# Optimization experiments

Measured on AMD Instinct MI355X. Metric: run time of the kernel, lower is better.

The kernel has to match this reference:

```python
import jax, jax.numpy as jnp
import numpy as np

B = 64          # molecules per batch
N_ATOMS = 16    # atoms per molecule (uniform -> torch.split == reshape)
DIM = 128
N = B * N_ATOMS # 1024 total atoms
N_FP = 10000
N_BOND_FP = 10000
EPS = 1e-12     # F.normalize default eps


def setup_inputs() -> dict:
    key = jax.random.key(0)
    ks = jax.random.split(key, 12)
    s = 1.0 / np.sqrt(DIM)
    # block-diagonal structure: molecule id per atom
    mol = jnp.arange(N) // N_ATOMS
    block = mol[:, None] == mol[None, :]
    fingerprints = jax.random.randint(ks[0], (N,), 0, N_FP, dtype=jnp.int32)
    # pad() fills off-block with 0.0; in-block: sparse binary bonds
    adjacency = jnp.where(block, (jax.random.uniform(ks[1], (N, N)) < 0.3).astype(jnp.float32), 0.0)
    # pad_MPO() fills off-block with index 0 (which still embeds to a real row!)
    bond_index = jnp.where(block, jax.random.randint(ks[2], (N, N), 0, N_BOND_FP, dtype=jnp.int32), 0)
    return {
        "fingerprints": fingerprints,
        "adjacency": adjacency,
        "bond_index": bond_index,
        "E_fp": jax.random.normal(ks[3], (N_FP, DIM), jnp.float32),
        "E_bond": jax.random.normal(ks[4], (N_BOND_FP, DIM), jnp.float32),
        "W_fp": jax.random.normal(ks[5], (DIM, DIM), jnp.float32) * s,
        "b_fp": jnp.zeros((DIM,), jnp.float32),
        "W_out0": jax.random.normal(ks[6], (DIM, DIM), jnp.float32) * s,
        "b_out0": jnp.zeros((DIM,), jnp.float32),
        "W_out1": jax.random.normal(ks[7], (DIM, DIM), jnp.float32) * s,
        "b_out1": jnp.zeros((DIM,), jnp.float32),
        "W_prop": jax.random.normal(ks[8], (DIM, 1), jnp.float32) * s,
        "b_prop": jnp.zeros((1,), jnp.float32),
    }


def _l2norm(x, axis):
    n = jnp.sqrt(jnp.sum(x * x, axis=axis, keepdims=True))
    return x / jnp.maximum(n, EPS)


def reference(fingerprints, adjacency, bond_index, E_fp, E_bond, W_fp, b_fp,
              W_out0, b_out0, W_out1, b_out1, W_prop, b_prop):
    # MPS: atom embeddings + one round of dense (block-diag) message passing
    mps = E_fp[fingerprints]                                   # [N, d]
    contri = jax.nn.relu(mps @ W_fp + b_fp)                    # [N, d]
    mps = mps + adjacency @ contri                             # [N, d]
    mps = _l2norm(mps, axis=1)                                 # F.normalize(., 2, 1)
    # MPO: embedding of the padded [N, N] bond index -> [N, N, d]
    mpo = E_bond[bond_index]                                   # [N, N, d]
    mpo = _l2norm(mpo, axis=1)                                 # normalize over 2nd atom axis
    # tmp[c, b] = sum_a mps[a, c] * mpo[a, b, c]
    tmp = jnp.einsum('ac,abc->cb', mps, mpo)                   # [d, N]
    # uniform molecular_sizes -> torch.split == reshape
    info = tmp.reshape(DIM, B, N_ATOMS)                        # [d, B, n]
    fv = mps.reshape(B, N_ATOMS, DIM)                          # [B, n, d]
    tn = jnp.einsum('dmn,mnd->md', info, fv)                   # [B, d]
    x = jax.nn.relu(tn @ W_out0 + b_out0)
    x = jax.nn.relu(x @ W_out1 + b_out1)
    return x @ W_prop + b_prop                                 # [B, 1]
```

## Files before the change

### kernel.cpp

```cpp
#include <hip/hip_runtime.h>
#include <math.h>

#define DIM_   128
#define NAT_   16
#define NTOT_  1024
#define BMOL_  64
#define OFFB_  1008.0f
#define EPSF_  1e-12f

__global__ __launch_bounds__(1024) void kA(const int* __restrict__ fp,
                                           const float* __restrict__ Efp,
                                           const float* __restrict__ Wfp,
                                           const float* __restrict__ bfp,
                                           const float* __restrict__ adj,
                                           const int* __restrict__ bidx,
                                           const float* __restrict__ Ebond,
                                           float* __restrict__ TnP_g,
                                           float* __restrict__ SbP_g,
                                           float* __restrict__ Mb_g) {
    const int b = blockIdx.x;
    const int m = b >> 1, h = b & 1, base = m * NAT_;
    const int t = threadIdx.x;
    const int c = t & 127;
    const int s = t >> 7;
    const int j0 = 2 * s, j1 = 2 * s + 1;
    const int jg = 8 * h + s;

    __shared__ float mpsS[NAT_][DIM_];
    __shared__ float conS[NAT_][DIM_];
    __shared__ float adjS[NAT_][NAT_];
    __shared__ int   bSh[8][NAT_];
    __shared__ float redS[NAT_][2];
    __shared__ float nrmS[NAT_];
    __shared__ float sb8[8][DIM_];
    __shared__ float tnp8[8][DIM_];

    {
        int j = t >> 7, cc = t & 127;
        mpsS[j][cc] = Efp[(size_t)fp[base + j] * DIM_ + cc];
        j += 8;
        mpsS[j][cc] = Efp[(size_t)fp[base + j] * DIM_ + cc];
    }
    if (t < 256) {
        const int j = t >> 4, i = t & 15;
        adjS[j][i] = adj[(size_t)(base + j) * NTOT_ + base + i];
    } else if (t < 384) {
        const int tt = t - 256, j = tt >> 4, i = tt & 15;
        bSh[j][i] = bidx[(size_t)(base + 8 * h + j) * NTOT_ + base + i];
    }
    __syncthreads();

    float a0 = bfp[c];
    float a1 = a0;
    #pragma unroll 8
    for (int k = 0; k < DIM_; ++k) {
        const float w = Wfp[(size_t)k * DIM_ + c];
        a0 += mpsS[j0][k] * w;
        a1 += mpsS[j1][k] * w;
    }
    conS[j0][c] = fmaxf(a0, 0.0f);
    conS[j1][c] = fmaxf(a1, 0.0f);
    __syncthreads();

    float ms0 = mpsS[j0][c], ms1 = mpsS[j1][c];
    #pragma unroll
    for (int i = 0; i < NAT_; ++i) {
        const float cv = conS[i][c];
        ms0 += adjS[j0][i] * cv;
        ms1 += adjS[j1][i] * cv;
    }
    float v0 = ms0 * ms0, v1 = ms1 * ms1;
    #pragma unroll
    for (int o = 32; o > 0; o >>= 1) {
        v0 += __shfl_xor(v0, o, 64);
        v1 += __shfl_xor(v1, o, 64);
    }
    const int half = (t >> 6) & 1;
    if ((t & 63) == 0) { redS[j0][half] = v0; redS[j1][half] = v1; }
    __syncthreads();
    if (t < NAT_) nrmS[t] = fmaxf(sqrtf(redS[t][0] + redS[t][1]), EPSF_);
    __syncthreads();
    mpsS[j0][c] = ms0 / nrmS[j0];
    mpsS[j1][c] = ms1 / nrmS[j1];
    __syncthreads();

    {
        const float e0 = Ebond[c];
        float nsq = OFFB_ * e0 * e0;
        int bb[NAT_];
        #pragma unroll
        for (int i = 0; i < NAT_; ++i) bb[i] = bSh[s][i];
        float ev[NAT_];
        #pragma unroll
        for (int i = 0; i < NAT_; ++i) ev[i] = Ebond[(size_t)bb[i] * DIM_ + c];
        #pragma unroll
        for (int i = 0; i < NAT_; ++i) nsq += ev[i] * ev[i];
        const float msc = mpsS[jg][c] / fmaxf(sqrtf(nsq), EPSF_);
        float tj = 0.0f;
        #pragma unroll
        for (int i = 0; i < NAT_; ++i) tj += ev[i] * mpsS[i][c];
        sb8[s][c]  = msc;
        tnp8[s][c] = msc * tj;
    }
    __syncthreads();

    if (s == 0) {
        float Tn = 0.0f, Sb = 0.0f;
        #pragma unroll
        for (int q = 0; q < 8; ++q) { Tn += tnp8[q][c]; Sb += sb8[q][c]; }
        TnP_g[(size_t)b * DIM_ + c] = Tn;
        SbP_g[(size_t)b * DIM_ + c] = Sb;
    } else if (s == 1 && h == 0) {
        float mb = 0.0f;
        #pragma unroll
        for (int i = 0; i < NAT_; ++i) mb += mpsS[i][c];
        Mb_g[(size_t)m * DIM_ + c] = mb;
    }
}

__global__ __launch_bounds__(512) void kB(const float* __restrict__ Ebond,
                                          const float* __restrict__ TnP_g,
                                          const float* __restrict__ SbP_g,
                                          const float* __restrict__ Mb_g,
                                          const float* __restrict__ W0, const float* __restrict__ b0,
                                          const float* __restrict__ W1, const float* __restrict__ b1,
                                          const float* __restrict__ Wp, const float* __restrict__ bp,
                                          float* __restrict__ out) {
    const int m = blockIdx.x;
    const int t = threadIdx.x;
    const int c = t & 127;
    const int s = t >> 7;
    __shared__ float w4[4][DIM_];
    __shared__ float vS[DIM_];
    __shared__ float tnS[DIM_];
    __shared__ float r2[2];

    {
        float S = 0.0f;
        float tv[32];
        #pragma unroll
        for (int r = 0; r < 32; ++r)
            tv[r] = SbP_g[(size_t)(s * 32 + r) * DIM_ + c];
        #pragma unroll
        for (int r = 0; r < 32; ++r) S += tv[r];
        w4[s][c] = S;
    }
    __syncthreads();
    if (s == 0) {
        const float Sall = w4[0][c] + w4[1][c] + w4[2][c] + w4[3][c];
        const float Sb_m = SbP_g[(size_t)(2 * m) * DIM_ + c] + SbP_g[(size_t)(2 * m + 1) * DIM_ + c];
        const float Tn_m = TnP_g[(size_t)(2 * m) * DIM_ + c] + TnP_g[(size_t)(2 * m + 1) * DIM_ + c];
        vS[c] = Tn_m + Ebond[c] * (Sall - Sb_m) * Mb_g[(size_t)m * DIM_ + c];
    }
    __syncthreads();

    {
        float a1 = 0.0f;
        #pragma unroll 8
        for (int r = 0; r < 32; ++r) {
            const int d = s * 32 + r;
            a1 += vS[d] * W0[(size_t)d * DIM_ + c];
        }
        w4[s][c] = a1;
    }
    __syncthreads();
    if (s == 0) tnS[c] = fmaxf(w4[0][c] + w4[1][c] + w4[2][c] + w4[3][c] + b0[c], 0.0f);
    __syncthreads();
    {
        float a2 = 0.0f;
        #pragma unroll 8
        for (int r = 0; r < 32; ++r) {
            const int d = s * 32 + r;
            a2 += tnS[d] * W1[(size_t)d * DIM_ + c];
        }
        w4[s][c] = a2;
    }
    __syncthreads();
    if (s == 0) {
        const float x1 = fmaxf(w4[0][c] + w4[1][c] + w4[2][c] + w4[3][c] + b1[c], 0.0f);
        float vv = x1 * Wp[c];
        #pragma unroll
        for (int o = 32; o > 0; o >>= 1) vv += __shfl_xor(vv, o, 64);
        if ((c & 63) == 0) r2[c >> 6] = vv;
    }
    __syncthreads();
    if (t == 0) out[m] = r2[0] + r2[1] + bp[0];
}

extern "C" void kernel_launch(void* const* d_in, const int* in_sizes, int n_in,
                              void* d_out, int out_size, void* d_ws, size_t ws_size,
                              hipStream_t stream) {
    const int*   fingerprints = (const int*)  d_in[0];
    const float* adjacency    = (const float*)d_in[1];
    const int*   bond_index   = (const int*)  d_in[2];
    const float* E_fp         = (const float*)d_in[3];
    const float* E_bond       = (const float*)d_in[4];
    const float* W_fp         = (const float*)d_in[5];
    const float* b_fp         = (const float*)d_in[6];
    const float* W_out0       = (const float*)d_in[7];
    const float* b_out0       = (const float*)d_in[8];
    const float* W_out1       = (const float*)d_in[9];
    const float* b_out1       = (const float*)d_in[10];
    const float* W_prop       = (const float*)d_in[11];
    const float* b_prop       = (const float*)d_in[12];
    float* out = (float*)d_out;

    float* ws = (float*)d_ws;
    const size_t PD = (size_t)128 * DIM_;
    float* TnP = ws;
    float* SbP = ws + PD;
    float* Mb  = ws + 2 * PD;

    kA<<<128, 1024, 0, stream>>>(fingerprints, E_fp, W_fp, b_fp, adjacency, bond_index,
                                 E_bond, TnP, SbP, Mb);
    kB<<<BMOL_, 512, 0, stream>>>(E_bond, TnP, SbP, Mb,
                                  W_out0, b_out0, W_out1, b_out1, W_prop, b_prop, out);
}
```

Before: 18.53 us.

## Split kA into compute and gather warp groups to overlap bond gather with MPS

The 1024-thread block is split into two halves. The upper 512 threads load bond indices and gather the E_bond rows, computing their squared norms while the lower 512 threads run the W_fp matmul, adjacency message passing and normalization, each thread handling four atoms with float4 LDS reads. The intent is to hide the latency of the random E_bond gathers behind the MPS compute instead of running the two serially. In exchange, the gather threads hold 32 loaded values in registers across barriers, which raises register pressure, and each half of the block now does twice the per-thread work.

New measurement: 19.09 us. +3.1%, slower.

```diff
diff --git a/kernel.cpp b/kernel.cpp
--- a/kernel.cpp
+++ b/kernel.cpp
@@ -22,99 +22,137 @@
     const int m = b >> 1, h = b & 1, base = m * NAT_;
     const int t = threadIdx.x;
     const int c = t & 127;
-    const int s = t >> 7;
-    const int j0 = 2 * s, j1 = 2 * s + 1;
-    const int jg = 8 * h + s;
+    const bool isGather = (t >= 512);
 
     __shared__ float mpsS[NAT_][DIM_];
     __shared__ float conS[NAT_][DIM_];
     __shared__ float adjS[NAT_][NAT_];
-    __shared__ int   bSh[8][NAT_];
     __shared__ float redS[NAT_][2];
     __shared__ float nrmS[NAT_];
     __shared__ float sb8[8][DIM_];
     __shared__ float tnp8[8][DIM_];
 
     {
-        int j = t >> 7, cc = t & 127;
-        mpsS[j][cc] = Efp[(size_t)fp[base + j] * DIM_ + cc];
-        j += 8;
-        mpsS[j][cc] = Efp[(size_t)fp[base + j] * DIM_ + cc];
+        const int j = t >> 7;
+        mpsS[j][c]     = Efp[(size_t)fp[base + j]     * DIM_ + c];
+        mpsS[j + 8][c] = Efp[(size_t)fp[base + j + 8] * DIM_ + c];
     }
     if (t < 256) {
         const int j = t >> 4, i = t & 15;
         adjS[j][i] = adj[(size_t)(base + j) * NTOT_ + base + i];
-    } else if (t < 384) {
-        const int tt = t - 256, j = tt >> 4, i = tt & 15;
-        bSh[j][i] = bidx[(size_t)(base + 8 * h + j) * NTOT_ + base + i];
-    }
-    __syncthreads();
-
-    float a0 = bfp[c];
-    float a1 = a0;
-    #pragma unroll 8
-    for (int k = 0; k < DIM_; ++k) {
-        const float w = Wfp[(size_t)k * DIM_ + c];
-        a0 += mpsS[j0][k] * w;
-        a1 += mpsS[j1][k] * w;
-    }
-    conS[j0][c] = fmaxf(a0, 0.0f);
-    conS[j1][c] = fmaxf(a1, 0.0f);
-    __syncthreads();
-
-    float ms0 = mpsS[j0][c], ms1 = mpsS[j1][c];
-    #pragma unroll
-    for (int i = 0; i < NAT_; ++i) {
-        const float cv = conS[i][c];
-        ms0 += adjS[j0][i] * cv;
-        ms1 += adjS[j1][i] * cv;
-    }
-    float v0 = ms0 * ms0, v1 = ms1 * ms1;
-    #pragma unroll
-    for (int o = 32; o > 0; o >>= 1) {
-        v0 += __shfl_xor(v0, o, 64);
-        v1 += __shfl_xor(v1, o, 64);
-    }
-    const int half = (t >> 6) & 1;
-    if ((t & 63) == 0) { redS[j0][half] = v0; redS[j1][half] = v1; }
+    }
+
+    int bb0[NAT_], bb1[NAT_];
+    const int g = (t - 512) >> 7;
+    const int jg0 = 8 * h + 2 * g, jg1 = jg0 + 1;
+    if (isGather) {
+        const size_t r0 = (size_t)(base + jg0) * NTOT_ + base;
+        const size_t r1 = (size_t)(base + jg1) * NTOT_ + base;
+        #pragma unroll
+        for (int i = 0; i < NAT_; ++i) bb0[i] = bidx[r0 + i];
+        #pragma unroll
+        for (int i = 0; i < NAT_; ++i) bb1[i] = bidx[r1 + i];
+    }
+    __syncthreads();
+
+    float ev0[NAT_], ev1[NAT_];
+    float nsq0 = 0.0f, nsq1 = 0.0f;
+    float msv[4];
+    const int q = t >> 7;
+
+    if (isGather) {
+        #pragma unroll
+        for (int i = 0; i < NAT_; ++i) ev0[i] = Ebond[(size_t)bb0[i] * DIM_ + c];
+        #pragma unroll
+        for (int i = 0; i < NAT_; ++i) ev1[i] = Ebond[(size_t)bb1[i] * DIM_ + c];
+        const float e0 = Ebond[c];
+        nsq0 = nsq1 = OFFB_ * e0 * e0;
+        #pragma unroll
+        for (int i = 0; i < NAT_; ++i) { nsq0 += ev0[i] * ev0[i]; nsq1 += ev1[i] * ev1[i]; }
+    } else {
+        float acc0 = bfp[c], acc1 = acc0, acc2 = acc0, acc3 = acc0;
+        #pragma unroll 4
+        for (int k = 0; k < DIM_; k += 4) {
+            const float4 m0 = *reinterpret_cast<const float4*>(&mpsS[4 * q + 0][k]);
+            const float4 m1 = *reinterpret_cast<const float4*>(&mpsS[4 * q + 1][k]);
+            const float4 m2 = *reinterpret_cast<const float4*>(&mpsS[4 * q + 2][k]);
+            const float4 m3 = *reinterpret_cast<const float4*>(&mpsS[4 * q + 3][k]);
+            const float w0 = Wfp[(size_t)(k + 0) * DIM_ + c];
+            const float w1 = Wfp[(size_t)(k + 1) * DIM_ + c];
+            const float w2 = Wfp[(size_t)(k + 2) * DIM_ + c];
+            const float w3 = Wfp[(size_t)(k + 3) * DIM_ + c];
+            acc0 += m0.x * w0 + m0.y * w1 + m0.z * w2 + m0.w * w3;
+            acc1 += m1.x * w0 + m1.y * w1 + m1.z * w2 + m1.w * w3;
+            acc2 += m2.x * w0 + m2.y * w1 + m2.z * w2 + m2.w * w3;
+            acc3 += m3.x * w0 + m3.y * w1 + m3.z * w2 + m3.w * w3;
+        }
+        conS[4 * q + 0][c] = fmaxf(acc0, 0.0f);
+        conS[4 * q + 1][c] = fmaxf(acc1, 0.0f);
+        conS[4 * q + 2][c] = fmaxf(acc2, 0.0f);
+        conS[4 * q + 3][c] = fmaxf(acc3, 0.0f);
+    }
+    __syncthreads();
+
+    if (!isGather) {
+        #pragma unroll
+        for (int jj = 0; jj < 4; ++jj) {
+            const int j = 4 * q + jj;
+            float x = mpsS[j][c];
+            #pragma unroll
+            for (int i = 0; i < NAT_; ++i) x += adjS[j][i] * conS[i][c];
+            msv[jj] = x;
+            float v = x * x;
+            #pragma unroll
+            for (int o = 32; o > 0; o >>= 1) v += __shfl_xor(v, o, 64);
+            if ((t & 63) == 0) redS[j][(t >> 6) & 1] = v;
+        }
+    }
     __syncthreads();
     if (t < NAT_) nrmS[t] = fmaxf(sqrtf(redS[t][0] + redS[t][1]), EPSF_);
     __syncthreads();
-    mpsS[j0][c] = ms0 / nrmS[j0];
-    mpsS[j1][c] = ms1 / nrmS[j1];
-    __syncthreads();
-
-    {
-        const float e0 = Ebond[c];
-        float nsq = OFFB_ * e0 * e0;
-        int bb[NAT_];
-        #pragma unroll
-        for (int i = 0; i < NAT_; ++i) bb[i] = bSh[s][i];
-        float ev[NAT_];
-        #pragma unroll
-        for (int i = 0; i < NAT_; ++i) ev[i] = Ebond[(size_t)bb[i] * DIM_ + c];
-        #pragma unroll
-        for (int i = 0; i < NAT_; ++i) nsq += ev[i] * ev[i];
-        const float msc = mpsS[jg][c] / fmaxf(sqrtf(nsq), EPSF_);
-        float tj = 0.0f;
-        #pragma unroll
-        for (int i = 0; i < NAT_; ++i) tj += ev[i] * mpsS[i][c];
-        sb8[s][c]  = msc;
-        tnp8[s][c] = msc * tj;
-    }
-    __syncthreads();
-
-    if (s == 0) {
-        float Tn = 0.0f, Sb = 0.0f;
-        #pragma unroll
-        for (int q = 0; q < 8; ++q) { Tn += tnp8[q][c]; Sb += sb8[q][c]; }
-        TnP_g[(size_t)b * DIM_ + c] = Tn;
-        SbP_g[(size_t)b * DIM_ + c] = Sb;
-    } else if (s == 1 && h == 0) {
-        float mb = 0.0f;
-        #pragma unroll
-        for (int i = 0; i < NAT_; ++i) mb += mpsS[i][c];
-        Mb_g[(size_t)m * DIM_ + c] = mb;
+    if (!isGather) {
+        #pragma unroll
+        for (int jj = 0; jj < 4; ++jj) {
+            const int j = 4 * q + jj;
+            mpsS[j][c] = msv[jj] / nrmS[j];
+        }
+    }
+    __syncthreads();
+
+    if (isGather) {
+        const float msc0 = mpsS[jg0][c] / fmaxf(sqrtf(nsq0), EPSF_);
+        const float msc1 = mpsS[jg1][c] / fmaxf(sqrtf(nsq1), EPSF_);
+        float tj0 = 0.0f, tj1 = 0.0f;
+        #pragma unroll
+        for (int i = 0; i < NAT_; ++i) {
+            const float mi = mpsS[i][c];
+            tj0 += ev0[i] * mi;
+            tj1 += ev1[i] * mi;
+        }
+        sb8[2 * g + 0][c]  = msc0;
+        sb8[2 * g + 1][c]  = msc1;
+        tnp8[2 * g + 0][c] = msc0 * tj0;
+        tnp8[2 * g + 1][c] = msc1 * tj1;
+    }
+    __syncthreads();
+
+    if (t < 128) {
+        float v = 0.0f;
+        #pragma unroll
+        for (int r = 0; r < 8; ++r) v += sb8[r][t];
+        SbP_g[(size_t)b * DIM_ + t] = v;
+    } else if (t < 256) {
+        const int cc = t - 128;
+        float v = 0.0f;
+        #pragma unroll
+        for (int r = 0; r < 8; ++r) v += tnp8[r][cc];
+        TnP_g[(size_t)b * DIM_ + cc] = v;
+    } else if (t < 384 && h == 0) {
+        const int cc = t - 256;
+        float v = 0.0f;
+        #pragma unroll
+        for (int j = 0; j < NAT_; ++j) v += mpsS[j][cc];
+        Mb_g[(size_t)m * DIM_ + cc] = v;
     }
 }
 
```
